# Kernel optimization log

Hardware: AMD Instinct MI355X
Metric: run time of the kernel (lower is better)

Reference implementation:

```python
import jax, jax.numpy as jnp
import numpy as np

B, T, D, H = 2, 4096, 768, 12
DH = D // H


def setup_inputs() -> dict:
    key = jax.random.key(0)
    ks = jax.random.split(key, 4)
    x = jax.random.normal(ks[0], (B, T, D), dtype=jnp.float32)
    Wqkv = jax.random.normal(ks[1], (D, 3 * D), dtype=jnp.float32) * (D ** -0.5)
    bqkv = jnp.zeros((3 * D,), dtype=jnp.float32)
    Wproj = jax.random.normal(ks[2], (D, D), dtype=jnp.float32) * (D ** -0.5)
    bproj = jnp.zeros((D,), dtype=jnp.float32)
    return {"x": x, "Wqkv": Wqkv, "bqkv": bqkv, "Wproj": Wproj, "bproj": bproj}


def reference(x, Wqkv, bqkv, Wproj, bproj):
    b, t, c = x.shape
    qkv = x @ Wqkv + bqkv                      # [B,T,3D]
    qkv = qkv.reshape(b, t, H, 3 * DH)
    q, k, v = jnp.split(qkv, 3, axis=-1)       # each [B,T,H,DH]
    q = q.transpose(0, 2, 1, 3)                # [B,H,T,DH]
    k = k.transpose(0, 2, 1, 3)
    v = v.transpose(0, 2, 1, 3)
    att = jnp.einsum('bhqd,bhkd->bhqk', q, k) / (DH ** 0.5)  # [B,H,T,T]
    mask = jnp.tril(jnp.ones((t, t), dtype=bool))
    att = jnp.where(mask, att, jnp.float32(-1e9))
    att = jax.nn.softmax(att, axis=-1)
    out = jnp.einsum('bhqk,bhkd->bhqd', att, v)  # [B,H,T,DH]
    out = out.transpose(0, 2, 1, 3).reshape(b, t, c)
    return out @ Wproj + bproj
```

## Files before the change

### kernel.cpp

```cpp
#include <hip/hip_runtime.h>

typedef unsigned short u16;
typedef unsigned int u32;
typedef __bf16 bf16x8 __attribute__((ext_vector_type(8)));
typedef float f32x4 __attribute__((ext_vector_type(4)));
typedef float f32x16 __attribute__((ext_vector_type(16)));
typedef u16 u16x4 __attribute__((ext_vector_type(4)));
typedef u16 u16x8 __attribute__((ext_vector_type(8)));
typedef u32 u32x2 __attribute__((ext_vector_type(2)));
typedef u32 u32x4 __attribute__((ext_vector_type(4)));

#define QSCALE 0.18033688011112042f
#define MFIX 12.0f

static __device__ __forceinline__ u16 f2bf(float f) {
  __bf16 h = (__bf16)f;
  return __builtin_bit_cast(u16, h);
}

static __device__ __forceinline__ u32 pk2(float a, float b) {
  return (u32)f2bf(a) | ((u32)f2bf(b) << 16);
}

static __device__ __forceinline__ void gl_lds16(const void* g, void* l) {
  __builtin_amdgcn_global_load_lds(
      (const __attribute__((address_space(1))) unsigned int*)g,
      (__attribute__((address_space(3))) unsigned int*)l, 16, 0, 0);
}

static __device__ __forceinline__ void wait_vmcnt4() {
  asm volatile("s_waitcnt vmcnt(4)" ::: "memory");
}
static __device__ __forceinline__ void wait_vmcnt2() {
  asm volatile("s_waitcnt vmcnt(2)" ::: "memory");
}
static __device__ __forceinline__ void wait_vmcnt0() {
  asm volatile("s_waitcnt vmcnt(0)" ::: "memory");
}
static __device__ __forceinline__ void barrier_mem() {
  asm volatile("s_barrier" ::: "memory");
}

static __device__ __forceinline__ f32x16 zero16() {
  f32x16 z;
#pragma unroll
  for (int i = 0; i < 16; ++i) z[i] = 0.f;
  return z;
}

__global__ void k_cvt(const float* __restrict__ in, u16* __restrict__ out, int n4) {
  int i = blockIdx.x * 256 + threadIdx.x;
  if (i < n4) {
    f32x4 f = ((const f32x4*)in)[i];
    u16x4 u = { f2bf(f[0]), f2bf(f[1]), f2bf(f[2]), f2bf(f[3]) };
    ((u16x4*)out)[i] = u;
  }
}

__global__ void k_transpose_cvt(const float* __restrict__ in, u16* __restrict__ out,
                                int R, int C) {
  __shared__ float tile[32][33];
  const int c0 = blockIdx.x * 32, r0 = blockIdx.y * 32;
  const int tx = threadIdx.x, ty = threadIdx.y;
#pragma unroll
  for (int i = 0; i < 4; ++i)
    tile[ty + i * 8][tx] = in[(size_t)(r0 + ty + i * 8) * C + c0 + tx];
  __syncthreads();
#pragma unroll
  for (int i = 0; i < 4; ++i)
    out[(size_t)(c0 + ty + i * 8) * R + r0 + tx] = f2bf(tile[tx][ty + i * 8]);
}

static __device__ __forceinline__ void gemm_core(const u16* __restrict__ Ag,
                                                 const u16* __restrict__ Btg,
                                                 int K, int m0, int n0,
                                                 u16* As, u16* Bs,
                                                 f32x4 acc[4][4]) {
  const int tid = threadIdx.x;
  const int lane = tid & 63;
  const int wid = tid >> 6;
  const int wm = wid >> 1, wn = wid & 1;
  const int l16 = lane & 15, lg = lane >> 4;

  for (int kt = 0; kt < K; kt += 64) {
    __syncthreads();
#pragma unroll
    for (int i = 0; i < 4; ++i) {
      int chunk = i * 256 + tid;
      int row = chunk >> 3;
      int lcb = ((chunk & 7) << 4) ^ ((row & 7) << 4);
      gl_lds16(Ag + (size_t)(m0 + row) * K + kt + (lcb >> 1),
               As + ((i * 256 + wid * 64) << 3));
    }
#pragma unroll
    for (int i = 0; i < 4; ++i) {
      int chunk = i * 256 + tid;
      int row = chunk >> 3;
      int lcb = ((chunk & 7) << 4) ^ ((row & 7) << 4);
      gl_lds16(Btg + (size_t)(n0 + row) * K + kt + (lcb >> 1),
               Bs + ((i * 256 + wid * 64) << 3));
    }
    __syncthreads();

#pragma unroll
    for (int ks = 0; ks < 2; ++ks) {
      bf16x8 af[4], bfr[4];
#pragma unroll
      for (int mi = 0; mi < 4; ++mi) {
        int row = wm * 64 + mi * 16 + l16;
        int off = row * 128 + ((ks * 64 + (lg << 4)) ^ ((row & 7) << 4));
        af[mi] = *(const bf16x8*)((const char*)As + off);
      }
#pragma unroll
      for (int ni = 0; ni < 4; ++ni) {
        int row = wn * 64 + ni * 16 + l16;
        int off = row * 128 + ((ks * 64 + (lg << 4)) ^ ((row & 7) << 4));
        bfr[ni] = *(const bf16x8*)((const char*)Bs + off);
      }
#pragma unroll
      for (int mi = 0; mi < 4; ++mi)
#pragma unroll
        for (int ni = 0; ni < 4; ++ni)
          acc[mi][ni] = __builtin_amdgcn_mfma_f32_16x16x32_bf16(
              af[mi], bfr[ni], acc[mi][ni], 0, 0, 0);
    }
  }
}

__global__ __launch_bounds__(256) void k_gemm_qkv(
    const u16* __restrict__ A, const u16* __restrict__ Bt,
    const float* __restrict__ bias, u16* __restrict__ Q, u16* __restrict__ Kb,
    u16* __restrict__ Vt) {
  __shared__ __align__(16) u16 SH[128 * 128];
  u16* As = SH;
  u16* Bs = SH + 128 * 64;
  const int m0 = blockIdx.y * 128, n0 = blockIdx.x * 128;
  const f32x4 fz = {0.f, 0.f, 0.f, 0.f};
  f32x4 acc[4][4];
#pragma unroll
  for (int mi = 0; mi < 4; ++mi)
#pragma unroll
    for (int ni = 0; ni < 4; ++ni) acc[mi][ni] = fz;

  gemm_core(A, Bt, 768, m0, n0, As, Bs, acc);
  __syncthreads();

  const int tid = threadIdx.x, lane = tid & 63, wid = tid >> 6;
  const int wm = wid >> 1, wn = wid & 1, l16 = lane & 15, lg = lane >> 4;
#pragma unroll
  for (int mi = 0; mi < 4; ++mi)
#pragma unroll
    for (int ni = 0; ni < 4; ++ni) {
      int nl = wn * 64 + ni * 16 + l16;
      int n = n0 + nl;
      float bi = bias[n];
      int h = n / 192;
      int rr = n - h * 192;
      int ml = wm * 64 + mi * 16 + lg * 4;
      if (rr >= 128) {
        int m0w = m0 + ml;
        int bb = m0w >> 12, t0 = m0w & 4095;
        u16x4 vv;
#pragma unroll
        for (int r = 0; r < 4; ++r) vv[r] = f2bf(acc[mi][ni][r] + bi);
        *(u16x4*)(Vt + ((size_t)(bb * 12 + h) * 64 + (rr - 128)) * 4096 + t0) = vv;
      } else {
        float sc = (rr < 64) ? QSCALE : 1.0f;
#pragma unroll
        for (int r = 0; r < 4; ++r)
          SH[(ml + r) * 128 + nl] = f2bf((acc[mi][ni][r] + bi) * sc);
      }
    }
  __syncthreads();

  const int bb2 = m0 >> 12, tb = m0 & 4095;
#pragma unroll
  for (int i = 0; i < 8; ++i) {
    int id = i * 256 + tid;
    int row = id >> 4;
    int c = id & 15;
    int n = n0 + c * 8;
    int h = n / 192;
    int rr = n - h * 192;
    if (rr < 128) {
      u16x8 v = *(const u16x8*)(SH + row * 128 + c * 8);
      size_t base = ((size_t)(bb2 * 12 + h) * 4096 + tb + row) * 64;
      u16* dst = (rr < 64) ? (Q + base + rr) : (Kb + base + rr - 64);
      *(u16x8*)dst = v;
    }
  }
}

__global__ __launch_bounds__(256) void k_gemm_proj(
    const u16* __restrict__ A, const u16* __restrict__ Bt,
    const float* __restrict__ bias, float* __restrict__ out) {
  __shared__ __align__(16) u16 As[128 * 64];
  __shared__ __align__(16) u16 Bs[128 * 64];
  const int m0 = blockIdx.y * 128, n0 = blockIdx.x * 128;
  const f32x4 fz = {0.f, 0.f, 0.f, 0.f};
  f32x4 acc[4][4];
#pragma unroll
  for (int mi = 0; mi < 4; ++mi)
#pragma unroll
    for (int ni = 0; ni < 4; ++ni) acc[mi][ni] = fz;

  gemm_core(A, Bt, 768, m0, n0, As, Bs, acc);

  const int tid = threadIdx.x, lane = tid & 63, wid = tid >> 6;
  const int wm = wid >> 1, wn = wid & 1, l16 = lane & 15, lg = lane >> 4;
#pragma unroll
  for (int mi = 0; mi < 4; ++mi)
#pragma unroll
    for (int ni = 0; ni < 4; ++ni) {
      int n = n0 + wn * 64 + ni * 16 + l16;
      float bi = bias[n];
#pragma unroll
      for (int r = 0; r < 4; ++r) {
        int m = m0 + wm * 64 + mi * 16 + lg * 4 + r;
        out[(size_t)m * 768 + n] = acc[mi][ni][r] + bi;
      }
    }
}

__global__ __launch_bounds__(256, 4) void k_attn(const u16* __restrict__ Qg,
                                                 const u16* __restrict__ Kg,
                                                 const u16* __restrict__ Vtg,
                                                 u16* __restrict__ Og) {
  __shared__ __align__(16) u16 LDSB[12288];
  u16* const KsA = LDSB;
  u16* const KsB = LDSB + 4096;
  u16* const Vs = LDSB + 8192;
  const int bid = blockIdx.x;
  const int xcd = bid & 7;
  const int u = bid >> 3;
  const int s = u & 31;
  const int rnd = u >> 5;
  const int bh = xcd * 3 + (rnd >> 1);
  const int jX = (rnd & 1) ? s : (63 - s);
  const int tid = threadIdx.x;
  const int lane = tid & 63;
  const int wid = tid >> 6;
  const int qhalf = wid >> 1, khalf = wid & 1;
  const int l32 = lane & 31;
  const int hi = lane >> 5;
  const int rxor = (l32 & 7) << 4;
  const size_t qk_base = (size_t)bh * (4096 * 64);
  const size_t vt_base = (size_t)bh * (64 * 4096);
  const int b = bh / 12, h = bh - b * 12;

  const int qrow = jX * 64 + qhalf * 32 + l32;
  const int nkt = jX + 1;

  int coK[4];
#pragma unroll
  for (int st = 0; st < 4; ++st) coK[st] = (st * 32 + hi * 16) ^ rxor;
  int cvA[2], cvB[2];
#pragma unroll
  for (int kl = 0; kl < 2; ++kl) {
    int ks = 2 * khalf + kl;
    cvA[kl] = (ks * 32 + hi * 8) ^ rxor;
    cvB[kl] = (ks * 32 + 16 + hi * 8) ^ rxor;
  }
  const int rbK = (khalf * 32 + l32) * 128;
  const int rb0 = l32 * 128, rb1 = (32 + l32) * 128;

  const int trow = tid >> 3;
  const int tcol = ((((tid & 7) << 4) ^ ((trow & 7) << 4)) >> 1);
  const int tdst = tid << 3;
  const u16* kp0 = Kg + qk_base + (size_t)trow * 64 + tcol;
  const u16* kp1 = kp0 + (size_t)32 * 64;
  const u16* vq0 = Vtg + vt_base + (size_t)trow * 4096 + tcol;
  const u16* vq1 = vq0 + (size_t)32 * 4096;

  auto stageK = [&](u16* Kd) {
    gl_lds16(kp0, Kd + tdst);
    gl_lds16(kp1, Kd + 2048 + tdst);
    kp0 += 4096; kp1 += 4096;
  };
  auto stageV = [&]() {
    gl_lds16(vq0, Vs + tdst);
    gl_lds16(vq1, Vs + 2048 + tdst);
    vq0 += 64; vq1 += 64;
  };

  bf16x8 qb[4];
#pragma unroll
  for (int st = 0; st < 4; ++st)
    qb[st] = *(const bf16x8*)(Qg + qk_base + (size_t)qrow * 64 + st * 16 + hi * 8);

  f32x16 o0 = zero16(), o1 = zero16();
  float lrun = 0.f;

  stageK(KsA);

  for (int kt = 0; kt < nkt; ++kt) {
    const bool more = (kt + 1 < nkt);
    stageV();
    if (more) stageK((kt & 1) ? KsA : KsB);
    if (more) wait_vmcnt4(); else wait_vmcnt2();
    barrier_mem();

    const bool diag = (kt == nkt - 1);
    const bool skip = diag && (qhalf == 0) && (khalf == 1);
    const bool tri = diag && (qhalf == khalf);
    const char* Kbp = (const char*)((kt & 1) ? KsB : KsA);
    const char* Vb = (const char*)Vs;

    f32x16 s0 = zero16();
    if (!skip) {
      __builtin_amdgcn_s_setprio(1);
#pragma unroll
      for (int st = 0; st < 4; ++st) {
        bf16x8 ka = *(const bf16x8*)(Kbp + rbK + coK[st]);
        s0 = __builtin_amdgcn_mfma_f32_32x32x16_bf16(ka, qb[st], s0, 0, 0, 0);
      }
      __builtin_amdgcn_s_setprio(0);

      if (tri) {
        const int kbase = kt * 64 + khalf * 32 + 4 * hi;
#pragma unroll
        for (int r = 0; r < 16; ++r) {
          int kpv = kbase + (r & 3) + 8 * (r >> 2);
          s0[r] = (kpv > qrow) ? -3.0e38f : s0[r];
        }
      }

#pragma unroll
      for (int r = 0; r < 16; ++r)
        s0[r] = __builtin_amdgcn_exp2f(s0[r] - MFIX);

      float a4[4];
#pragma unroll
      for (int r = 0; r < 4; ++r)
        a4[r] = (s0[r] + s0[r + 4]) + (s0[r + 8] + s0[r + 12]);
      lrun += (a4[0] + a4[1]) + (a4[2] + a4[3]);
    }

    if (more) wait_vmcnt2(); else wait_vmcnt0();
    barrier_mem();

    if (!skip) {
      __builtin_amdgcn_s_setprio(1);
#pragma unroll
      for (int kl = 0; kl < 2; ++kl) {
        const int base = kl * 8;
        u32x4 w = { pk2(s0[base + 0], s0[base + 1]), pk2(s0[base + 2], s0[base + 3]),
                    pk2(s0[base + 4], s0[base + 5]), pk2(s0[base + 6], s0[base + 7]) };
        bf16x8 pbk = __builtin_bit_cast(bf16x8, w);
        u32x2 q0 = *(const u32x2*)(Vb + rb0 + cvA[kl]);
        u32x2 q1 = *(const u32x2*)(Vb + rb0 + cvB[kl]);
        u32x4 av = {q0[0], q0[1], q1[0], q1[1]};
        bf16x8 va0 = __builtin_bit_cast(bf16x8, av);
        o0 = __builtin_amdgcn_mfma_f32_32x32x16_bf16(va0, pbk, o0, 0, 0, 0);
        u32x2 p0 = *(const u32x2*)(Vb + rb1 + cvA[kl]);
        u32x2 p1 = *(const u32x2*)(Vb + rb1 + cvB[kl]);
        u32x4 bv = {p0[0], p0[1], p1[0], p1[1]};
        bf16x8 va1 = __builtin_bit_cast(bf16x8, bv);
        o1 = __builtin_amdgcn_mfma_f32_32x32x16_bf16(va1, pbk, o1, 0, 0, 0);
      }
      __builtin_amdgcn_s_setprio(0);
    }

    barrier_mem();
  }

  float* red = (float*)LDSB;
  if (khalf == 1) {
    float* dst = red + (qhalf * 64 + lane) * 33;
#pragma unroll
    for (int i = 0; i < 16; ++i) {
      dst[i] = o0[i];
      dst[16 + i] = o1[i];
    }
    dst[32] = lrun;
  }
  __syncthreads();
  if (khalf == 0) {
    const float* src = red + (qhalf * 64 + lane) * 33;
#pragma unroll
    for (int i = 0; i < 16; ++i) {
      o0[i] += src[i];
      o1[i] += src[16 + i];
    }
    lrun += src[32];
    float lt = lrun + __shfl_xor(lrun, 32, 64);
    float inv = 1.0f / lt;
    u16* orow = Og + ((size_t)b * 4096 + qrow) * 768 + h * 64;
#pragma unroll
    for (int gg = 0; gg < 4; ++gg) {
      u16x4 v0, v1;
#pragma unroll
      for (int i = 0; i < 4; ++i) {
        v0[i] = f2bf(o0[4 * gg + i] * inv);
        v1[i] = f2bf(o1[4 * gg + i] * inv);
      }
      *(u16x4*)(orow + 8 * gg + 4 * hi) = v0;
      *(u16x4*)(orow + 32 + 8 * gg + 4 * hi) = v1;
    }
  }
}

extern "C" void kernel_launch(void* const* d_in, const int* in_sizes, int n_in,
                              void* d_out, int out_size, void* d_ws, size_t ws_size,
                              hipStream_t stream) {
  const float* x = (const float*)d_in[0];
  const float* Wqkv = (const float*)d_in[1];
  const float* bqkv = (const float*)d_in[2];
  const float* Wproj = (const float*)d_in[3];
  const float* bproj = (const float*)d_in[4];
  float* out = (float*)d_out;

  char* ws = (char*)d_ws;
  u16* Xbf = (u16*)(ws + 0);
  u16* WqkvT = (u16*)(ws + 12582912);
  u16* WprojT = (u16*)(ws + 16121856);
  u16* Q = (u16*)(ws + 17301504);
  u16* K = (u16*)(ws + 29884416);
  u16* Vt = (u16*)(ws + 42467328);
  u16* O = (u16*)(ws + 55050240);

  k_cvt<<<6144, 256, 0, stream>>>(x, Xbf, 1572864);
  k_transpose_cvt<<<dim3(72, 24), dim3(32, 8), 0, stream>>>(Wqkv, WqkvT, 768, 2304);
  k_transpose_cvt<<<dim3(24, 24), dim3(32, 8), 0, stream>>>(Wproj, WprojT, 768, 768);
  k_gemm_qkv<<<dim3(18, 64), 256, 0, stream>>>(Xbf, WqkvT, bqkv, Q, K, Vt);
  k_attn<<<1536, 256, 0, stream>>>(Q, K, Vt, O);
  k_gemm_proj<<<dim3(6, 64), 256, 0, stream>>>(O, WprojT, bproj, out);
}
```

Baseline: 182.5 us.

## Double-buffer both K and V tiles with one barrier per iteration

The attention loop now double-buffers V alongside K, growing the LDS footprint from 24KB to 32KB per block. The next K/V tile is prefetched right after a single full wait and barrier. This removes the mid-iteration V wait, the second barrier, and the trailing barrier, so each iteration has one sync point instead of three. The trade-off is that each iteration waits for all outstanding loads (vmcnt 0) before computing, and the extra LDS may limit how many blocks fit per CU.

```diff
diff --git a/kernel.cpp b/kernel.cpp
--- a/kernel.cpp
+++ b/kernel.cpp
@@ -28,12 +28,6 @@
       (__attribute__((address_space(3))) unsigned int*)l, 16, 0, 0);
 }
 
-static __device__ __forceinline__ void wait_vmcnt4() {
-  asm volatile("s_waitcnt vmcnt(4)" ::: "memory");
-}
-static __device__ __forceinline__ void wait_vmcnt2() {
-  asm volatile("s_waitcnt vmcnt(2)" ::: "memory");
-}
 static __device__ __forceinline__ void wait_vmcnt0() {
   asm volatile("s_waitcnt vmcnt(0)" ::: "memory");
 }
@@ -226,10 +220,7 @@
                                                  const u16* __restrict__ Kg,
                                                  const u16* __restrict__ Vtg,
                                                  u16* __restrict__ Og) {
-  __shared__ __align__(16) u16 LDSB[12288];
-  u16* const KsA = LDSB;
-  u16* const KsB = LDSB + 4096;
-  u16* const Vs = LDSB + 8192;
+  __shared__ __align__(16) u16 LDSB[16384];
   const int bid = blockIdx.x;
   const int xcd = bid & 7;
   const int u = bid >> 3;
@@ -272,14 +263,14 @@
   const u16* vq0 = Vtg + vt_base + (size_t)trow * 4096 + tcol;
   const u16* vq1 = vq0 + (size_t)32 * 4096;
 
-  auto stageK = [&](u16* Kd) {
+  auto stage = [&](int buf) {
+    u16* Kd = LDSB + (buf << 12);
+    u16* Vd = LDSB + 8192 + (buf << 12);
     gl_lds16(kp0, Kd + tdst);
     gl_lds16(kp1, Kd + 2048 + tdst);
+    gl_lds16(vq0, Vd + tdst);
+    gl_lds16(vq1, Vd + 2048 + tdst);
     kp0 += 4096; kp1 += 4096;
-  };
-  auto stageV = [&]() {
-    gl_lds16(vq0, Vs + tdst);
-    gl_lds16(vq1, Vs + 2048 + tdst);
     vq0 += 64; vq1 += 64;
   };
 
@@ -291,20 +282,18 @@
   f32x16 o0 = zero16(), o1 = zero16();
   float lrun = 0.f;
 
-  stageK(KsA);
+  stage(0);
 
   for (int kt = 0; kt < nkt; ++kt) {
-    const bool more = (kt + 1 < nkt);
-    stageV();
-    if (more) stageK((kt & 1) ? KsA : KsB);
-    if (more) wait_vmcnt4(); else wait_vmcnt2();
+    wait_vmcnt0();
     barrier_mem();
+    if (kt + 1 < nkt) stage((kt + 1) & 1);
 
     const bool diag = (kt == nkt - 1);
     const bool skip = diag && (qhalf == 0) && (khalf == 1);
     const bool tri = diag && (qhalf == khalf);
-    const char* Kbp = (const char*)((kt & 1) ? KsB : KsA);
-    const char* Vb = (const char*)Vs;
+    const char* Kbp = (const char*)(LDSB + ((kt & 1) << 12));
+    const char* Vb = (const char*)(LDSB + 8192 + ((kt & 1) << 12));
 
     f32x16 s0 = zero16();
     if (!skip) {
@@ -334,12 +323,7 @@
       for (int r = 0; r < 4; ++r)
         a4[r] = (s0[r] + s0[r + 4]) + (s0[r + 8] + s0[r + 12]);
       lrun += (a4[0] + a4[1]) + (a4[2] + a4[3]);
-    }
-
-    if (more) wait_vmcnt2(); else wait_vmcnt0();
-    barrier_mem();
-
-    if (!skip) {
+
       __builtin_amdgcn_s_setprio(1);
 #pragma unroll
       for (int kl = 0; kl < 2; ++kl) {
@@ -360,10 +344,9 @@
       }
       __builtin_amdgcn_s_setprio(0);
     }
-
-    barrier_mem();
-  }
-
+  }
+
+  __syncthreads();
   float* red = (float*)LDSB;
   if (khalf == 1) {
     float* dst = red + (qhalf * 64 + lane) * 33;
```

Measured after the change: 183.1 us. Within noise of the previous version (+0.3%).
